# Optimization experiments

Measured on AMD Instinct MI355X. Metric: run time of the kernel, lower is better.

## Reference

```python
import jax, jax.numpy as jnp
import numpy as np

GROUP_SIZE = 64  # init_kwargs: group_size
BATCH = 1024
NEURONS = 65536  # must be divisible by GROUP_SIZE


def setup_inputs() -> dict:
    key = jax.random.key(0)
    kx, kp = jax.random.split(key)
    # positive activations (firing rates) so group sums are nonzero
    x = jax.random.uniform(kx, (BATCH, NEURONS), dtype=jnp.float32)
    # build()'s np.random.shuffle(np.arange(neuron_num)) -> fixed random permutation
    index = jax.random.permutation(kp, jnp.arange(NEURONS, dtype=jnp.int32))
    return {"x": x, "index": index}


def reference(x, index):
    # x: [B, N] activations; index: [N] permutation defining group membership.
    # Group g = permuted neurons [g*GROUP_SIZE, (g+1)*GROUP_SIZE).
    B, N = x.shape
    gathered = x[:, index].reshape(B, N // GROUP_SIZE, GROUP_SIZE)  # [B, G, gs]
    norm = gathered / jnp.sum(gathered, axis=-1, keepdims=True)     # divisive normalization
    # scatter back to original neuron positions: out[:, index] = norm
    out = jnp.zeros_like(x).at[:, index].set(norm.reshape(B, N))
    return out
```

## Files before the change

### kernel.cpp

```cpp
#include <hip/hip_runtime.h>
#include <hip/hip_bf16.h>

#define BATCH   1024
#define NEUR    65536
#define NGRP    1024
#define BLK     1024
#define NCHUNK  4
#define CHUNK   (NEUR / NCHUNK)
#define CHUNK_F4 (CHUNK / 4)
#define F4T     (CHUNK_F4 / BLK)
#define KMAX    24
#define SENT    CHUNK
#define ROW_F4  (NEUR / 4)
#define HALF_F4 (ROW_F4 / 2)
#define H_ITERS (HALF_F4 / BLK)
#define BUCKET_ELEMS (NCHUNK * NGRP * KMAX)
#define SPILL_CAP 1024
#define NSUM    (BATCH * NGRP)

typedef float          f32x4  __attribute__((ext_vector_type(4)));
typedef unsigned short u16x8  __attribute__((ext_vector_type(8)));


__global__ void init_tables(unsigned short* __restrict__ bucket,
                            unsigned int* __restrict__ spill) {
    int i = blockIdx.x * blockDim.x + threadIdx.x;
    if (i < BUCKET_ELEMS) bucket[i] = (unsigned short)SENT;
    if (i == 0) spill[0] = 0;
}

__global__ void build_tables(const int* __restrict__ index,
                             int* __restrict__ group_of,
                             unsigned short* __restrict__ bucket,
                             unsigned int* __restrict__ spill) {
    const int p    = blockIdx.x * blockDim.x + threadIdx.x;
    const int lane = threadIdx.x & 63;
    const int g    = p >> 6;
    const int s    = index[p];
    group_of[s] = g;
    const int c = s / CHUNK;
    unsigned long long mc = 0;
    #pragma unroll
    for (int cc = 0; cc < NCHUNK; ++cc) {
        unsigned long long m = __ballot(c == cc);
        if (cc == c) mc = m;
    }
    const int k = __popcll(mc & ((1ull << lane) - 1ull));
    if (k < KMAX) {
        bucket[((size_t)(c * NGRP + g)) * KMAX + k] = (unsigned short)(s & (CHUNK - 1));
    } else {
        unsigned int pos = atomicAdd(spill, 1u);
        if (pos < SPILL_CAP - 1)
            spill[1 + pos] = ((unsigned)g << 16) | (unsigned)s;
    }
}

__global__ __launch_bounds__(BLK, 8)
void k1_partial(const float* __restrict__ x,
                const unsigned short* __restrict__ bucket,
                float* __restrict__ part) {
    __shared__ float xs[CHUNK + 16];
    const int bc = blockIdx.x;
    const int b  = bc >> 2;
    const int c  = bc & 3;
    const int t  = threadIdx.x;

    if (t == 0) xs[SENT] = 0.0f;

    const float4* __restrict__ src =
        (const float4*)(x + (size_t)b * NEUR + (size_t)c * CHUNK);
    #pragma unroll
    for (int i = 0; i < F4T; ++i) ((float4*)xs)[i * BLK + t] = src[i * BLK + t];
    __syncthreads();

    const unsigned short* __restrict__ bk =
        bucket + ((size_t)(c * NGRP + t)) * KMAX;
    const u16x8 w0 = *(const u16x8*)(bk);
    const u16x8 w1 = *(const u16x8*)(bk + 8);
    const u16x8 w2 = *(const u16x8*)(bk + 16);

    float a0 = 0.0f, a1 = 0.0f;
    #pragma unroll
    for (int j = 0; j < 8; ++j) {
        a0 += xs[w0[j]];
        a1 += xs[w1[j]];
        a0 += xs[w2[j]];
    }
    part[(size_t)c * NSUM + b * NGRP + t] = a0 + a1;
}

__global__ __launch_bounds__(BLK, 8)
void k3_scale(const float* __restrict__ x,
              const int* __restrict__ group_of,
              const float* __restrict__ part,
              const unsigned int* __restrict__ spill,
              float* __restrict__ out) {
    __shared__ float rsum[NGRP];
    const int rb   = blockIdx.x;
    const int b    = (BATCH - 1) - (rb >> 1);
    const int half = rb & 1;
    const int t    = threadIdx.x;
    const float* __restrict__ xrow = x + (size_t)b * NEUR;

    float s = part[0 * NSUM + b * NGRP + t]
            + part[1 * NSUM + b * NGRP + t]
            + part[2 * NSUM + b * NGRP + t]
            + part[3 * NSUM + b * NGRP + t];
    const unsigned int ns = spill[0];
    for (unsigned int e = 0; e < ns; ++e) {
        const unsigned int ent = spill[1 + e];
        if ((int)(ent >> 16) == t) s += xrow[ent & 0xFFFFu];
    }
    rsum[t] = 1.0f / s;
    __syncthreads();

    const float4* __restrict__ xrow4 = (const float4*)xrow;
    const int4*   __restrict__ gof4  = (const int4*)group_of;
    f32x4*        __restrict__ orow4 = (f32x4*)(out + (size_t)b * NEUR);

    #pragma unroll
    for (int it = 0; it < H_ITERS; ++it) {
        const int e = half * HALF_F4 + it * BLK + t;
        const float4 v = xrow4[e];
        const int4  g = gof4[e];
        f32x4 o;
        o.x = v.x * rsum[g.x];
        o.y = v.y * rsum[g.y];
        o.z = v.z * rsum[g.z];
        o.w = v.w * rsum[g.w];
        __builtin_nontemporal_store(o, &orow4[e]);
    }
}

extern "C" void kernel_launch(void* const* d_in, const int* in_sizes, int n_in,
                              void* d_out, int out_size, void* d_ws, size_t ws_size,
                              hipStream_t stream) {
    const float* x     = (const float*)d_in[0];
    const int*   index = (const int*)d_in[1];
    float*       out   = (float*)d_out;

    int*            group_of = (int*)d_ws;
    unsigned short* bucket   = (unsigned short*)(group_of + NEUR);
    float*          part     = (float*)(bucket + BUCKET_ELEMS);
    unsigned int*   spill    = (unsigned int*)(part + NCHUNK * NSUM);

    init_tables<<<BUCKET_ELEMS / BLK, BLK, 0, stream>>>(bucket, spill);
    build_tables<<<NEUR / BLK, BLK, 0, stream>>>(index, group_of, bucket, spill);
    k1_partial<<<BATCH * NCHUNK, BLK, 0, stream>>>(x, bucket, part);
    k3_scale<<<BATCH * 2, BLK, 0, stream>>>(x, group_of, part, spill, out);
}
```

Measured before the change: 158.1 us.

## Shrink group table to u16, move spill handling into partial kernel, split rows in quarters

Stores the group-of table as 16-bit indices instead of 32-bit, which halves that gather-table traffic in the scale pass. Spill entries are now added from shared memory inside the partial-sum kernel, so the scale kernel no longer loops over the spill list. Partial sums are laid out per row so each row's four chunk sums sit together. The scale kernel now launches four blocks per row instead of two, giving more parallelism at the cost of recomputing the reciprocal sums in more blocks.

```diff
diff --git a/kernel.cpp b/kernel.cpp
--- a/kernel.cpp
+++ b/kernel.cpp
@@ -12,14 +12,15 @@
 #define KMAX    24
 #define SENT    CHUNK
 #define ROW_F4  (NEUR / 4)
-#define HALF_F4 (ROW_F4 / 2)
-#define H_ITERS (HALF_F4 / BLK)
+#define Q_F4    (ROW_F4 / 4)
+#define Q_ITERS (Q_F4 / BLK)
 #define BUCKET_ELEMS (NCHUNK * NGRP * KMAX)
 #define SPILL_CAP 1024
 #define NSUM    (BATCH * NGRP)
 
-typedef float          f32x4  __attribute__((ext_vector_type(4)));
-typedef unsigned short u16x8  __attribute__((ext_vector_type(8)));
+typedef float          f32x4 __attribute__((ext_vector_type(4)));
+typedef unsigned short u16x8 __attribute__((ext_vector_type(8)));
+typedef unsigned short u16x4 __attribute__((ext_vector_type(4)));
 
 
 __global__ void init_tables(unsigned short* __restrict__ bucket,
@@ -30,14 +31,14 @@
 }
 
 __global__ void build_tables(const int* __restrict__ index,
-                             int* __restrict__ group_of,
+                             unsigned short* __restrict__ gof,
                              unsigned short* __restrict__ bucket,
                              unsigned int* __restrict__ spill) {
     const int p    = blockIdx.x * blockDim.x + threadIdx.x;
     const int lane = threadIdx.x & 63;
     const int g    = p >> 6;
     const int s    = index[p];
-    group_of[s] = g;
+    gof[s] = (unsigned short)g;
     const int c = s / CHUNK;
     unsigned long long mc = 0;
     #pragma unroll
@@ -58,6 +59,7 @@
 __global__ __launch_bounds__(BLK, 8)
 void k1_partial(const float* __restrict__ x,
                 const unsigned short* __restrict__ bucket,
+                const unsigned int* __restrict__ spill,
                 float* __restrict__ part) {
     __shared__ float xs[CHUNK + 16];
     const int bc = blockIdx.x;
@@ -86,43 +88,42 @@
         a1 += xs[w1[j]];
         a0 += xs[w2[j]];
     }
-    part[(size_t)c * NSUM + b * NGRP + t] = a0 + a1;
+
+    const unsigned int ns = spill[0];
+    for (unsigned int e = 0; e < ns; ++e) {
+        const unsigned int ent = spill[1 + e];
+        if ((int)(ent >> 16) == t && (int)((ent >> 14) & 3u) == c)
+            a1 += xs[ent & 0x3FFFu];
+    }
+
+    part[((size_t)b * NCHUNK + c) * NGRP + t] = a0 + a1;
 }
 
 __global__ __launch_bounds__(BLK, 8)
 void k3_scale(const float* __restrict__ x,
-              const int* __restrict__ group_of,
+              const unsigned short* __restrict__ gof,
               const float* __restrict__ part,
-              const unsigned int* __restrict__ spill,
               float* __restrict__ out) {
     __shared__ float rsum[NGRP];
-    const int rb   = blockIdx.x;
-    const int b    = (BATCH - 1) - (rb >> 1);
-    const int half = rb & 1;
-    const int t    = threadIdx.x;
-    const float* __restrict__ xrow = x + (size_t)b * NEUR;
+    const int rb = blockIdx.x;
+    const int b  = (BATCH - 1) - (rb >> 2);
+    const int q  = rb & 3;
+    const int t  = threadIdx.x;
 
-    float s = part[0 * NSUM + b * NGRP + t]
-            + part[1 * NSUM + b * NGRP + t]
-            + part[2 * NSUM + b * NGRP + t]
-            + part[3 * NSUM + b * NGRP + t];
-    const unsigned int ns = spill[0];
-    for (unsigned int e = 0; e < ns; ++e) {
-        const unsigned int ent = spill[1 + e];
-        if ((int)(ent >> 16) == t) s += xrow[ent & 0xFFFFu];
-    }
+    const float* __restrict__ prow = part + (size_t)b * NCHUNK * NGRP;
+    float s = prow[t] + prow[NGRP + t] + prow[2 * NGRP + t] + prow[3 * NGRP + t];
     rsum[t] = 1.0f / s;
     __syncthreads();
 
-    const float4* __restrict__ xrow4 = (const float4*)xrow;
-    const int4*   __restrict__ gof4  = (const int4*)group_of;
+    const float4* __restrict__ xrow4 = (const float4*)(x + (size_t)b * NEUR);
+    const u16x4*  __restrict__ gof4  = (const u16x4*)gof;
     f32x4*        __restrict__ orow4 = (f32x4*)(out + (size_t)b * NEUR);
 
     #pragma unroll
-    for (int it = 0; it < H_ITERS; ++it) {
-        const int e = half * HALF_F4 + it * BLK + t;
+    for (int it = 0; it < Q_ITERS; ++it) {
+        const int e = q * Q_F4 + it * BLK + t;
         const float4 v = xrow4[e];
-        const int4  g = gof4[e];
+        const u16x4 g = gof4[e];
         f32x4 o;
         o.x = v.x * rsum[g.x];
         o.y = v.y * rsum[g.y];
@@ -139,13 +140,13 @@
     const int*   index = (const int*)d_in[1];
     float*       out   = (float*)d_out;
 
-    int*            group_of = (int*)d_ws;
-    unsigned short* bucket   = (unsigned short*)(group_of + NEUR);
-    float*          part     = (float*)(bucket + BUCKET_ELEMS);
-    unsigned int*   spill    = (unsigned int*)(part + NCHUNK * NSUM);
+    unsigned short* gof    = (unsigned short*)d_ws;
+    unsigned short* bucket = gof + NEUR;
+    float*          part   = (float*)(bucket + BUCKET_ELEMS);
+    unsigned int*   spill  = (unsigned int*)(part + (size_t)BATCH * NCHUNK * NGRP);
 
     init_tables<<<BUCKET_ELEMS / BLK, BLK, 0, stream>>>(bucket, spill);
-    build_tables<<<NEUR / BLK, BLK, 0, stream>>>(index, group_of, bucket, spill);
-    k1_partial<<<BATCH * NCHUNK, BLK, 0, stream>>>(x, bucket, part);
-    k3_scale<<<BATCH * 2, BLK, 0, stream>>>(x, group_of, part, spill, out);
+    build_tables<<<NEUR / BLK, BLK, 0, stream>>>(index, gof, bucket, spill);
+    k1_partial<<<BATCH * NCHUNK, BLK, 0, stream>>>(x, bucket, spill, part);
+    k3_scale<<<BATCH * 4, BLK, 0, stream>>>(x, gof, part, out);
 }
```

Measured after the change: 165.2 us. +4.5%, slower.
